# Kernel optimization log

Measured on AMD Instinct MI355X. Metric: run time of the kernel, lower is better.

## Reference

```python
import math
import jax, jax.numpy as jnp
import numpy as np

D_MODEL = 256
NUM_HEAD = 8
NUM_LEVEL = 1
KERNEL = 5
NUM_POINT = KERNEL * KERNEL
NUM_VAR = 5  # with_rotation=True
HEAD_DIM = D_MODEL // NUM_HEAD


def _kernel_indices(k=KERNEL):
    # odd kernel: linspace(-(k-1)/2, (k-1)/2, k); torch.meshgrid default 'ij'; stack([j,i])/k
    idx = jnp.linspace(-(k - 1) / 2.0, (k - 1) / 2.0, k)
    ii, jj = jnp.meshgrid(idx, idx, indexing='ij')
    return jnp.stack([jj, ii], axis=-1).reshape(-1, 2) / k  # (P, 2)


def setup_inputs() -> dict:
    key = jax.random.key(0)
    ks = jax.random.split(key, 8)
    B, LQ = 2, 4096
    Hf, Wf = 188, 188
    LV = Hf * Wf
    d = D_MODEL
    nb = NUM_LEVEL * NUM_HEAD * NUM_VAR
    na = NUM_HEAD * NUM_LEVEL * NUM_POINT
    return {
        'query': jax.random.normal(ks[0], (B, LQ, d), jnp.float32),
        'value': jax.random.normal(ks[1], (B, LV, d), jnp.float32),
        'ref_windows': jax.random.uniform(ks[2], (B, LQ, 7), jnp.float32),
        'W_box': jax.random.normal(ks[3], (nb, d), jnp.float32) * 0.02,
        'b_box': jax.random.uniform(ks[4], (nb,), jnp.float32),
        'W_attn': jax.random.normal(ks[5], (na, d), jnp.float32) * 0.02,
        'b_attn': jnp.zeros((na,), jnp.float32),
        'W_value': jax.random.normal(ks[6], (d, d), jnp.float32) * 0.02,
        'b_value': jnp.zeros((d,), jnp.float32),
        'W_out': jax.random.normal(ks[7], (d, d), jnp.float32) * 0.02,
        'b_out': jnp.zeros((d,), jnp.float32),
        'H_feat': Hf,
        'W_feat': Wf,
    }


def reference(query, value, ref_windows, W_box, b_box, W_attn, b_attn,
              W_value, b_value, W_out, b_out, H_feat, W_feat):
    B, LQ, d = query.shape
    LV = value.shape[1]
    Hh, Lv, P, Dh = NUM_HEAD, NUM_LEVEL, NUM_POINT, HEAD_DIM

    # value projection -> (B, LV, Hh, Dh)
    v = (value @ W_value.T + b_value).reshape(B, LV, Hh, Dh)

    # attention weights: softmax over (level*point) per head
    attn = jax.nn.softmax((query @ W_attn.T + b_attn).reshape(B, LQ, Hh, Lv * P), axis=-1)
    attn = attn.reshape(B, LQ, Hh, Lv, P)

    # --- _where_to_attend ---
    ob = (query @ W_box.T + b_box).reshape(B, LQ, Hh, Lv, NUM_VAR)
    rw = ref_windows[:, :, None, None, :]                    # (B,LQ,1,1,7)
    ref_boxes = rw[..., jnp.array([0, 1, 3, 4])]             # cx, cy, w, h
    ref_angles = rw[..., 6:7]
    off_boxes, off_angles = ob[..., :4], ob[..., 4:5]
    angles = (ref_angles + off_angles / 16.0) * (2.0 * math.pi)
    boxes = ref_boxes + off_boxes / 8.0 * ref_boxes[..., jnp.array([2, 3, 2, 3])]
    center = boxes[..., None, :2]                            # (B,LQ,Hh,Lv,1,2)
    size = boxes[..., None, 2:4]
    cos_a, sin_a = jnp.cos(angles), jnp.sin(angles)
    rot = jnp.stack([cos_a, -sin_a, sin_a, cos_a], axis=-1).reshape(B, LQ, Hh, Lv, 1, 2, 2)
    g = _kernel_indices() * jax.nn.relu(size)                # (B,LQ,Hh,Lv,P,2)
    grid = center + (g[..., None, :] * rot).sum(-1)          # (B,LQ,Hh,Lv,P,2), normalized [0,1]

    # --- single-level bilinear sampling (align_corners=False, zero padding) ---
    gl = grid[:, :, :, 0]                                    # (B,LQ,Hh,P,2)
    gx = gl[..., 0] * W_feat - 0.5
    gy = gl[..., 1] * H_feat - 0.5
    x0 = jnp.floor(gx)
    y0 = jnp.floor(gy)
    x0i = x0.astype(jnp.int32)
    y0i = y0.astype(jnp.int32)
    wx1 = gx - x0
    wy1 = gy - y0
    wx0 = 1.0 - wx1
    wy0 = 1.0 - wy1

    b_idx = jnp.arange(B)[:, None, None, None]
    h_idx = jnp.arange(Hh)[None, None, :, None]

    def gather(yi, xi):
        valid = (xi >= 0) & (xi < W_feat) & (yi >= 0) & (yi < H_feat)
        lin = jnp.clip(yi, 0, H_feat - 1) * W_feat + jnp.clip(xi, 0, W_feat - 1)
        return v[b_idx, lin, h_idx] * valid[..., None]       # (B,LQ,Hh,P,Dh)

    s = (gather(y0i, x0i) * (wy0 * wx0)[..., None]
         + gather(y0i, x0i + 1) * (wy0 * wx1)[..., None]
         + gather(y0i + 1, x0i) * (wy1 * wx0)[..., None]
         + gather(y0i + 1, x0i + 1) * (wy1 * wx1)[..., None])

    out_heads = (s * attn[:, :, :, 0, :, None]).sum(axis=3)  # (B,LQ,Hh,Dh)
    out = out_heads.reshape(B, LQ, Hh * Dh) @ W_out.T + b_out
    attn_w = attn.reshape(B, LQ, Hh, Lv, KERNEL, KERNEL)
    return out, attn_w
```

## Files before the change

kernel.cpp:

```cpp
#include <hip/hip_runtime.h>


typedef float floatx4 __attribute__((ext_vector_type(4)));
typedef short shortx8 __attribute__((ext_vector_type(8)));

static __device__ __forceinline__ unsigned short f2bf(float x) {
    unsigned int u = __float_as_uint(x);
    return (unsigned short)((u + 0x7fffu + ((u >> 16) & 1u)) >> 16);
}
static __device__ __forceinline__ unsigned int pack2(float a, float b) {
    return (unsigned int)f2bf(a) | ((unsigned int)f2bf(b) << 16);
}
static __device__ __forceinline__ void async16(const void* g, void* lds) {
    __builtin_amdgcn_global_load_lds(
        (const __attribute__((address_space(1))) unsigned int*)g,
        (__attribute__((address_space(3))) unsigned int*)lds, 16, 0, 0);
}

__global__ __launch_bounds__(256) void convert_kernel(
    const float* __restrict__ W_value, unsigned short* __restrict__ wvbf,
    const float* __restrict__ W_attn, const float* __restrict__ W_box,
    float* __restrict__ Wab,
    const float* __restrict__ W_out, unsigned short* __restrict__ wobf,
    const float* __restrict__ b_attn, const float* __restrict__ b_box,
    float* __restrict__ bab)
{
    const int blk = blockIdx.x, tid = threadIdx.x;
    if (blk < 16) {
        int base = blk * 1024 + tid;
#pragma unroll
        for (int k = 0; k < 4; ++k) {
            int j = base + k * 256;
            float4 f = ((const float4*)W_value)[j];
            ((uint2*)wvbf)[j] = make_uint2(pack2(f.x, f.y), pack2(f.z, f.w));
        }
    } else if (blk < 32) {
        int base = (blk - 16) * 1024 + tid;
#pragma unroll
        for (int k = 0; k < 4; ++k) {
            int j = base + k * 256;
            int row = j >> 6, col = (j & 63) * 4;
            float4 f;
            if (row < 200)      f = *(const float4*)(W_attn + (size_t)row * 256 + col);
            else if (row < 240) f = *(const float4*)(W_box + (size_t)(row - 200) * 256 + col);
            else                f = make_float4(0.f, 0.f, 0.f, 0.f);
            ((float4*)Wab)[j] = f;
        }
    } else if (blk < 48) {
        int base = (blk - 32) * 1024 + tid;
#pragma unroll
        for (int k = 0; k < 4; ++k) {
            int j = base + k * 256;
            float4 f = ((const float4*)W_out)[j];
            ((uint2*)wobf)[j] = make_uint2(pack2(f.x, f.y), pack2(f.z, f.w));
        }
    } else {
        bab[tid] = tid < 200 ? b_attn[tid] : (tid < 240 ? b_box[tid - 200] : 0.f);
    }
}

__global__ __launch_bounds__(512) void gemm_vproj(
    const float* __restrict__ A,
    const unsigned short* __restrict__ Bw,
    const float* __restrict__ bias,
    unsigned short* __restrict__ Vout, int M, int LV)
{
    __shared__ unsigned short Bres[256 * 256];
    __shared__ unsigned short As[2][64 * 64];
    const int tid = threadIdx.x;
    const int wv = tid >> 6, lane = tid & 63;
    const int lr = lane & 15, lq = lane >> 4;
    const int wm = wv & 1, wn = wv >> 1;
    const int rowA = tid >> 3;
    const int gA = tid & 7;
    const int gAsw = gA ^ (rowA & 7);

#pragma unroll
    for (int j = 0; j < 16; ++j) {
        int G = j * 512 + tid;
        int row = G >> 5, g = G & 31;
        async16(Bw + (size_t)row * 256 + (g ^ (row & 7)) * 8,
                (char*)Bres + j * 8192 + wv * 1024);
    }

    const int niter = (M + 63) / 64;
    const int stride = gridDim.x;

    int it0 = blockIdx.x;
    float4 pf0, pf1;
    {
        int ra = it0 * 64 + rowA; ra = ra < M ? ra : M - 1;
        const float* ap = A + (size_t)ra * 256 + gA * 8;
        pf0 = *(const float4*)ap; pf1 = *(const float4*)(ap + 4);
        uint4 pv = make_uint4(pack2(pf0.x, pf0.y), pack2(pf0.z, pf0.w),
                              pack2(pf1.x, pf1.y), pack2(pf1.z, pf1.w));
        *(uint4*)((char*)As[0] + rowA * 128 + gAsw * 16) = pv;
    }
    __syncthreads();

    int buf = 0;
    for (int it = it0; it < niter; it += stride) {
        const int m0 = it * 64;
        floatx4 acc[2][4];
#pragma unroll
        for (int i = 0; i < 2; ++i)
#pragma unroll
            for (int j = 0; j < 4; ++j) acc[i][j] = (floatx4){0.f, 0.f, 0.f, 0.f};

#pragma unroll
        for (int kc = 0; kc < 4; ++kc) {
            int nit = it, nkc = kc + 1;
            if (nkc == 4) { nkc = 0; nit = it + stride; if (nit >= niter) nit = it; }
            {
                int ra = nit * 64 + rowA; ra = ra < M ? ra : M - 1;
                const float* ap = A + (size_t)ra * 256 + nkc * 64 + gA * 8;
                pf0 = *(const float4*)ap; pf1 = *(const float4*)(ap + 4);
            }
#pragma unroll
            for (int kb = 0; kb < 2; ++kb) {
                shortx8 af[2], bfr[4];
#pragma unroll
                for (int t = 0; t < 2; ++t) {
                    int arow = wm * 32 + t * 16 + lr;
                    af[t] = *(const shortx8*)((const char*)As[buf] + arow * 128 +
                                              (((kb * 4 + lq) ^ (arow & 7)) * 16));
                }
#pragma unroll
                for (int t = 0; t < 4; ++t) {
                    int brow = wn * 64 + t * 16 + lr;
                    int gg = kc * 8 + kb * 4 + lq;
                    bfr[t] = *(const shortx8*)((const char*)Bres + brow * 512 +
                                               ((gg ^ (brow & 7)) * 16));
                }
#pragma unroll
                for (int ti = 0; ti < 2; ++ti)
#pragma unroll
                    for (int tj = 0; tj < 4; ++tj)
                        acc[ti][tj] = __builtin_amdgcn_mfma_f32_16x16x32_bf16(bfr[tj], af[ti], acc[ti][tj], 0, 0, 0);
            }
            {
                uint4 pv = make_uint4(pack2(pf0.x, pf0.y), pack2(pf0.z, pf0.w),
                                      pack2(pf1.x, pf1.y), pack2(pf1.z, pf1.w));
                *(uint4*)((char*)As[buf ^ 1] + rowA * 128 + gAsw * 16) = pv;
            }
            __syncthreads();
            buf ^= 1;
        }
#pragma unroll
        for (int ti = 0; ti < 2; ++ti) {
            int m = m0 + wm * 32 + ti * 16 + lr;
            if (m >= M) continue;
            int b = m >= LV ? 1 : 0;
            int lv = m - (b ? LV : 0);
#pragma unroll
            for (int tj = 0; tj < 4; ++tj) {
                int nb = wn * 64 + tj * 16 + lq * 4;
                float4 bv = *(const float4*)(bias + nb);
                int h = nb >> 5, dh = nb & 31;
                unsigned short* dst = Vout + ((size_t)(b * 8 + h) * LV + lv) * 32 + dh;
                *(uint2*)dst = make_uint2(pack2(acc[ti][tj][0] + bv.x, acc[ti][tj][1] + bv.y),
                                          pack2(acc[ti][tj][2] + bv.z, acc[ti][tj][3] + bv.w));
            }
        }
    }
}

__global__ __launch_bounds__(256) void gemm_nt_bias(
    const float* __restrict__ A, const float* __restrict__ W,
    const float* __restrict__ bias, float* __restrict__ C, int M)
{
    const int K = 256, N = 256;
    __shared__ float As[16][68];
    __shared__ float Bs[16][68];
    int tid = threadIdx.x;
    int tcol = tid & 15, trow = tid >> 4;
    int m0 = blockIdx.x * 64, n0 = blockIdx.y * 64;
    int lr = tid >> 2, lc = (tid & 3) << 2;
    float acc[4][4] = {};
    for (int k0 = 0; k0 < K; k0 += 16) {
        int arow = m0 + lr; if (arow > M - 1) arow = M - 1;
        float4 av = *(const float4*)(A + (size_t)arow * K + k0 + lc);
        float4 wv = *(const float4*)(W + (size_t)(n0 + lr) * K + k0 + lc);
        __syncthreads();
        As[lc + 0][lr] = av.x; As[lc + 1][lr] = av.y; As[lc + 2][lr] = av.z; As[lc + 3][lr] = av.w;
        Bs[lc + 0][lr] = wv.x; Bs[lc + 1][lr] = wv.y; Bs[lc + 2][lr] = wv.z; Bs[lc + 3][lr] = wv.w;
        __syncthreads();
#pragma unroll
        for (int k = 0; k < 16; ++k) {
            float4 a4 = *(const float4*)&As[k][trow << 2];
            float4 b4 = *(const float4*)&Bs[k][tcol << 2];
            float a[4] = {a4.x, a4.y, a4.z, a4.w};
            float bb[4] = {b4.x, b4.y, b4.z, b4.w};
#pragma unroll
            for (int i = 0; i < 4; i++)
#pragma unroll
                for (int j = 0; j < 4; j++) acc[i][j] += a[i] * bb[j];
        }
    }
#pragma unroll
    for (int i = 0; i < 4; i++) {
        int m = m0 + trow * 4 + i;
        if (m >= M) continue;
#pragma unroll
        for (int j = 0; j < 4; j++) {
            int n = n0 + tcol * 4 + j;
            C[(size_t)m * N + n] = acc[i][j] + bias[n];
        }
    }
}

__global__ __launch_bounds__(256) void decode_sample_kernel(
    const unsigned short* __restrict__ v,
    const float* __restrict__ logits,
    const float* __restrict__ ref_windows,
    float* __restrict__ attn_out,
    unsigned short* __restrict__ ohbf,
    const int* __restrict__ Hf_p, const int* __restrict__ Wf_p, int LV, int LQ)
{
    __shared__ float lg[8][32];
    __shared__ float rw[8][7];
    __shared__ float prm[8][6];
    __shared__ float mxinv[8][2];
    __shared__ uint4 pk[8][25][2];

    const int lin = blockIdx.y * 16 + blockIdx.x;
    const int nc = gridDim.y;
    const int seq = lin >> 3;
    const int c = seq % nc;
    const int s = (lin & 7) + ((seq / nc) << 3);
    const int b = s >> 3, h = s & 7;
    const int tid = threadIdx.x;
    const int Hf = *Hf_p, Wf = *Wf_p;
    const size_t mbase = (size_t)b * LQ + c * 8;

    if (tid < 240) {
        int qq = tid / 30, j = tid - qq * 30;
        int col = (j < 25) ? h * 25 + j : 200 + h * 5 + (j - 25);
        lg[qq][j] = logits[(mbase + qq) * 256 + col];
    }
    if (tid < 56) {
        int qq = tid / 7, k = tid - qq * 7;
        rw[qq][k] = ref_windows[(mbase + qq) * 7 + k];
    }
    __syncthreads();

    if (tid < 8) {
        int qq = tid;
        float mx = -1e30f;
#pragma unroll
        for (int p = 0; p < 25; p++) mx = fmaxf(mx, lg[qq][p]);
        float ssum = 0.f;
#pragma unroll
        for (int p = 0; p < 25; p++) ssum += expf(lg[qq][p] - mx);
        mxinv[qq][0] = mx; mxinv[qq][1] = 1.f / ssum;
        float cx = rw[qq][0] + lg[qq][25] * 0.125f * rw[qq][3];
        float cy = rw[qq][1] + lg[qq][26] * 0.125f * rw[qq][4];
        float bw = rw[qq][3] + lg[qq][27] * 0.125f * rw[qq][3];
        float bh = rw[qq][4] + lg[qq][28] * 0.125f * rw[qq][4];
        float ang = (rw[qq][6] + lg[qq][29] * 0.0625f) * 6.283185307179586f;
        prm[qq][0] = cx; prm[qq][1] = cy;
        prm[qq][2] = fmaxf(bw, 0.f); prm[qq][3] = fmaxf(bh, 0.f);
        prm[qq][4] = cosf(ang); prm[qq][5] = sinf(ang);
    }
    __syncthreads();

    if (tid < 200) {
        int qq = tid / 25, p = tid - qq * 25;
        float a = expf(lg[qq][p] - mxinv[qq][0]) * mxinv[qq][1];
        attn_out[(mbase + qq) * 200 + h * 25 + p] = a;
        int pi = p / 5, pj = p - pi * 5;
        float g0 = (float)(pj - 2) * 0.2f * prm[qq][2];
        float g1 = (float)(pi - 2) * 0.2f * prm[qq][3];
        float ca = prm[qq][4], sa = prm[qq][5];
        float gx = (prm[qq][0] + g0 * ca - g1 * sa) * (float)Wf - 0.5f;
        float gy = (prm[qq][1] + g0 * sa + g1 * ca) * (float)Hf - 0.5f;
        float x0f = floorf(gx), y0f = floorf(gy);
        int x0 = (int)x0f, y0 = (int)y0f;
        float wx1 = gx - x0f, wy1 = gy - y0f;
        float wx0 = 1.f - wx1, wy0 = 1.f - wy1;
        int y1 = y0 + 1;
        int bx; float wl, wr;
        if (x0 >= 0 && x0 <= Wf - 2)      { bx = x0;     wl = wx0; wr = wx1; }
        else if (x0 == -1)                { bx = 0;      wl = wx1; wr = 0.f; }
        else if (x0 == Wf - 1)            { bx = Wf - 2; wl = 0.f; wr = wx0; }
        else                              { bx = 0;      wl = 0.f; wr = 0.f; }
        float wy0v = (y0 >= 0 && y0 < Hf) ? wy0 : 0.f;
        float wy1v = (y1 >= 0 && y1 < Hf) ? wy1 : 0.f;
        int cy0 = min(max(y0, 0), Hf - 1), cy1 = min(max(y1, 0), Hf - 1);
        unsigned off0 = (unsigned)(cy0 * Wf + bx) * 16u;
        unsigned off1 = (unsigned)(cy1 * Wf + bx) * 16u;
        float aw0 = a * wy0v, aw1 = a * wy1v;
        pk[qq][p][0] = make_uint4(__float_as_uint(aw0 * wl), __float_as_uint(aw1 * wl), off0, off1);
        pk[qq][p][1] = make_uint4(__float_as_uint(aw0 * wr), __float_as_uint(aw1 * wr), off0, off1);
    }
    __syncthreads();

    const int qq = tid >> 5, l = tid & 31;
    const unsigned int* vw = (const unsigned int*)(v + (size_t)s * LV * 32);
    const uint4* pkp = &pk[qq][0][l >> 4];
    float e0 = 0.f, o0 = 0.f, e1 = 0.f, o1 = 0.f;
#pragma unroll
    for (int p = 0; p < 25; ++p) {
        uint4 t = pkp[2 * p];
        float w0 = __uint_as_float(t.x), w1 = __uint_as_float(t.y);
        unsigned u0 = vw[t.z + l];
        unsigned u1 = vw[t.w + l];
        e0 += w0 * __uint_as_float(u0 << 16);
        o0 += w0 * __uint_as_float(u0 & 0xffff0000u);
        e1 += w1 * __uint_as_float(u1 << 16);
        o1 += w1 * __uint_as_float(u1 & 0xffff0000u);
    }
    float a0 = e0 + e1, a1 = o0 + o1;
    a0 += __shfl_xor(a0, 16, 32);
    a1 += __shfl_xor(a1, 16, 32);
    if (l < 16)
        ((unsigned int*)ohbf)[(mbase + qq) * 128 + h * 16 + l] = pack2(a0, a1);
}

__global__ __launch_bounds__(256) void gemm_out(
    const unsigned short* __restrict__ Ab,
    const unsigned short* __restrict__ Bw,
    const float* __restrict__ bias,
    float* __restrict__ C, int M)
{
    constexpr int BM = 64;
    constexpr int NI = BM / 32, TI = BM / 32;
    __shared__ unsigned short As[2][BM * 64];
    __shared__ unsigned short Bs[2][128 * 64];
    const int tid = threadIdx.x;
    const int wv = tid >> 6, lane = tid & 63;
    const int lr = lane & 15, lq = lane >> 4;
    const int m0 = blockIdx.x * BM, n0 = blockIdx.y * 128;
    const int wm = wv & 1, wn = wv >> 1;
    const int srow = tid >> 3;
    const int colg = tid & 7;
    const int colgSw = colg ^ (srow & 7);

    floatx4 acc[TI][4];
#pragma unroll
    for (int i = 0; i < TI; ++i)
#pragma unroll
        for (int j = 0; j < 4; ++j) acc[i][j] = (floatx4){0.f, 0.f, 0.f, 0.f};

    auto compute = [&](const unsigned short* Acur, const unsigned short* Bcur) {
#pragma unroll
        for (int kb = 0; kb < 2; ++kb) {
            shortx8 af[TI], bfr[4];
#pragma unroll
            for (int t = 0; t < TI; ++t) {
                int arow = wm * (BM / 2) + t * 16 + lr;
                af[t] = *(const shortx8*)&Acur[arow * 64 + (((kb * 4 + lq) ^ (arow & 7)) * 8)];
            }
#pragma unroll
            for (int t = 0; t < 4; ++t) {
                int brow = wn * 64 + t * 16 + lr;
                bfr[t] = *(const shortx8*)&Bcur[brow * 64 + (((kb * 4 + lq) ^ (brow & 7)) * 8)];
            }
#pragma unroll
            for (int ti = 0; ti < TI; ++ti)
#pragma unroll
                for (int tj = 0; tj < 4; ++tj)
                    acc[ti][tj] = __builtin_amdgcn_mfma_f32_16x16x32_bf16(bfr[tj], af[ti], acc[ti][tj], 0, 0, 0);
        }
    };

#pragma unroll
    for (int i = 0; i < NI; ++i) {
        int ra = m0 + i * 32 + srow; ra = ra < M ? ra : M - 1;
        async16(Ab + (size_t)ra * 256 + colgSw * 8, (char*)As[0] + i * 4096 + wv * 1024);
    }
#pragma unroll
    for (int i = 0; i < 4; ++i) {
        int rb = n0 + i * 32 + srow;
        async16(Bw + (size_t)rb * 256 + colgSw * 8, (char*)Bs[0] + i * 4096 + wv * 1024);
    }
    __syncthreads();
    int cur = 0;
    for (int kc = 0; kc < 4; ++kc) {
        const int nk = (kc + 1) * 64;
        if (kc < 3) {
#pragma unroll
            for (int i = 0; i < NI; ++i) {
                int ra = m0 + i * 32 + srow; ra = ra < M ? ra : M - 1;
                async16(Ab + (size_t)ra * 256 + nk + colgSw * 8,
                        (char*)As[cur ^ 1] + i * 4096 + wv * 1024);
            }
#pragma unroll
            for (int i = 0; i < 4; ++i) {
                int rb = n0 + i * 32 + srow;
                async16(Bw + (size_t)rb * 256 + nk + colgSw * 8,
                        (char*)Bs[cur ^ 1] + i * 4096 + wv * 1024);
            }
        }
        compute(As[cur], Bs[cur]);
        __syncthreads();
        cur ^= 1;
    }
#pragma unroll
    for (int ti = 0; ti < TI; ++ti) {
        int m = m0 + wm * (BM / 2) + ti * 16 + lr;
        if (m >= M) continue;
        float* Crow = C + (size_t)m * 256;
#pragma unroll
        for (int tj = 0; tj < 4; ++tj) {
            int nb = n0 + wn * 64 + tj * 16 + lq * 4;
            float4 bv = *(const float4*)(bias + nb);
            float4 o = make_float4(acc[ti][tj][0] + bv.x, acc[ti][tj][1] + bv.y,
                                   acc[ti][tj][2] + bv.z, acc[ti][tj][3] + bv.w);
            *(float4*)(Crow + nb) = o;
        }
    }
}

extern "C" void kernel_launch(void* const* d_in, const int* in_sizes, int n_in,
                              void* d_out, int out_size, void* d_ws, size_t ws_size,
                              hipStream_t stream) {
    const float* query       = (const float*)d_in[0];
    const float* value       = (const float*)d_in[1];
    const float* ref_windows = (const float*)d_in[2];
    const float* W_box       = (const float*)d_in[3];
    const float* b_box       = (const float*)d_in[4];
    const float* W_attn      = (const float*)d_in[5];
    const float* b_attn      = (const float*)d_in[6];
    const float* W_value     = (const float*)d_in[7];
    const float* b_value     = (const float*)d_in[8];
    const float* W_out       = (const float*)d_in[9];
    const float* b_out       = (const float*)d_in[10];
    const int*   Hf          = (const int*)d_in[11];
    const int*   Wf          = (const int*)d_in[12];

    const int M1 = in_sizes[1] / 256;
    const int MQ = in_sizes[0] / 256;
    const int LQ = MQ / 2;
    const int LV = M1 / 2;

    unsigned short* Vout = (unsigned short*)d_ws;
    unsigned short* ohbf = Vout + (size_t)M1 * 256;
    unsigned short* wvbf = ohbf + (size_t)MQ * 256;
    unsigned short* wobf = wvbf + 65536;
    float* Wab       = (float*)(wobf + 65536);
    float* bab       = Wab + 65536;
    float* logits    = bab + 256;

    float* out0     = (float*)d_out;
    float* attn_out = out0 + (size_t)MQ * 256;

    convert_kernel<<<49, 256, 0, stream>>>(W_value, wvbf, W_attn, W_box, Wab,
                                           W_out, wobf, b_attn, b_box, bab);
    gemm_vproj<<<256, 512, 0, stream>>>(value, wvbf, b_value, Vout, M1, LV);
    dim3 g2(MQ / 64, 4);
    gemm_nt_bias<<<g2, 256, 0, stream>>>(query, Wab, bab, logits, MQ);
    decode_sample_kernel<<<dim3(16, LQ / 8), 256, 0, stream>>>(
        Vout, logits, ref_windows, attn_out, ohbf, Hf, Wf, LV, LQ);
    dim3 g4(MQ / 64, 2);
    gemm_out<<<g4, 256, 0, stream>>>(ohbf, wobf, b_out, out0, MQ);
}
```

Before: 216.4 us.

## Fuse logits GEMM into weight-prep kernel and widen value projection blocks to 1024 threads

The query logits GEMM now runs inside the weight-conversion kernel, reading W_attn/W_box directly with inline bias selection. This removes one launch and the intermediate Wab/bab buffers. The value-projection GEMM moves from 512 to 1024 threads per block, with each wave owning a 16-row slice and loading half as much A per thread. That raises the number of waves per block but lowers per-wave MFMA work and A-fragment reuse. Prep blocks are heterogeneous, and MQ is assumed to be 128 tiles of 64 rows.

New measurement: 220.2 us. No clear change (+1.8%).

```diff
diff --git a/kernel.cpp b/kernel.cpp
--- a/kernel.cpp
+++ b/kernel.cpp
@@ -17,49 +17,78 @@
         (__attribute__((address_space(3))) unsigned int*)lds, 16, 0, 0);
 }
 
-__global__ __launch_bounds__(256) void convert_kernel(
+__global__ __launch_bounds__(256) void prep_kernel(
+    const float* __restrict__ query,
+    const float* __restrict__ W_attn, const float* __restrict__ W_box,
+    const float* __restrict__ b_attn, const float* __restrict__ b_box,
+    float* __restrict__ logits, int MQ,
     const float* __restrict__ W_value, unsigned short* __restrict__ wvbf,
-    const float* __restrict__ W_attn, const float* __restrict__ W_box,
-    float* __restrict__ Wab,
-    const float* __restrict__ W_out, unsigned short* __restrict__ wobf,
-    const float* __restrict__ b_attn, const float* __restrict__ b_box,
-    float* __restrict__ bab)
+    const float* __restrict__ W_out, unsigned short* __restrict__ wobf)
 {
     const int blk = blockIdx.x, tid = threadIdx.x;
-    if (blk < 16) {
-        int base = blk * 1024 + tid;
+    if (blk < 512) {
+        const int K = 256, N = 256, M = MQ;
+        __shared__ float As[16][68];
+        __shared__ float Bs[16][68];
+        int tcol = tid & 15, trow = tid >> 4;
+        int m0 = (blk & 127) * 64, n0 = (blk >> 7) * 64;
+        int lr = tid >> 2, lc = (tid & 3) << 2;
+        float acc[4][4] = {};
+        for (int k0 = 0; k0 < K; k0 += 16) {
+            int arow = m0 + lr; if (arow > M - 1) arow = M - 1;
+            float4 av = *(const float4*)(query + (size_t)arow * K + k0 + lc);
+            int r = n0 + lr;
+            float4 wv;
+            if (r < 200)      wv = *(const float4*)(W_attn + (size_t)r * 256 + k0 + lc);
+            else if (r < 240) wv = *(const float4*)(W_box + (size_t)(r - 200) * 256 + k0 + lc);
+            else              wv = make_float4(0.f, 0.f, 0.f, 0.f);
+            __syncthreads();
+            As[lc + 0][lr] = av.x; As[lc + 1][lr] = av.y; As[lc + 2][lr] = av.z; As[lc + 3][lr] = av.w;
+            Bs[lc + 0][lr] = wv.x; Bs[lc + 1][lr] = wv.y; Bs[lc + 2][lr] = wv.z; Bs[lc + 3][lr] = wv.w;
+            __syncthreads();
+#pragma unroll
+            for (int k = 0; k < 16; ++k) {
+                float4 a4 = *(const float4*)&As[k][trow << 2];
+                float4 b4 = *(const float4*)&Bs[k][tcol << 2];
+                float a[4] = {a4.x, a4.y, a4.z, a4.w};
+                float bb[4] = {b4.x, b4.y, b4.z, b4.w};
+#pragma unroll
+                for (int i = 0; i < 4; i++)
+#pragma unroll
+                    for (int j = 0; j < 4; j++) acc[i][j] += a[i] * bb[j];
+            }
+        }
+#pragma unroll
+        for (int i = 0; i < 4; i++) {
+            int m = m0 + trow * 4 + i;
+            if (m >= M) continue;
+#pragma unroll
+            for (int j = 0; j < 4; j++) {
+                int n = n0 + tcol * 4 + j;
+                float bb = n < 200 ? b_attn[n] : (n < 240 ? b_box[n - 200] : 0.f);
+                logits[(size_t)m * N + n] = acc[i][j] + bb;
+            }
+        }
+    } else if (blk < 528) {
+        int base = (blk - 512) * 1024 + tid;
 #pragma unroll
         for (int k = 0; k < 4; ++k) {
             int j = base + k * 256;
             float4 f = ((const float4*)W_value)[j];
             ((uint2*)wvbf)[j] = make_uint2(pack2(f.x, f.y), pack2(f.z, f.w));
         }
-    } else if (blk < 32) {
-        int base = (blk - 16) * 1024 + tid;
-#pragma unroll
-        for (int k = 0; k < 4; ++k) {
-            int j = base + k * 256;
-            int row = j >> 6, col = (j & 63) * 4;
-            float4 f;
-            if (row < 200)      f = *(const float4*)(W_attn + (size_t)row * 256 + col);
-            else if (row < 240) f = *(const float4*)(W_box + (size_t)(row - 200) * 256 + col);
-            else                f = make_float4(0.f, 0.f, 0.f, 0.f);
-            ((float4*)Wab)[j] = f;
-        }
-    } else if (blk < 48) {
-        int base = (blk - 32) * 1024 + tid;
+    } else {
+        int base = (blk - 528) * 1024 + tid;
 #pragma unroll
         for (int k = 0; k < 4; ++k) {
             int j = base + k * 256;
             float4 f = ((const float4*)W_out)[j];
             ((uint2*)wobf)[j] = make_uint2(pack2(f.x, f.y), pack2(f.z, f.w));
         }
-    } else {
-        bab[tid] = tid < 200 ? b_attn[tid] : (tid < 240 ? b_box[tid - 200] : 0.f);
-    }
-}
-
-__global__ __launch_bounds__(512) void gemm_vproj(
+    }
+}
+
+__global__ __launch_bounds__(1024) void gemm_vproj(
     const float* __restrict__ A,
     const unsigned short* __restrict__ Bw,
     const float* __restrict__ bias,
@@ -70,42 +99,37 @@
     const int tid = threadIdx.x;
     const int wv = tid >> 6, lane = tid & 63;
     const int lr = lane & 15, lq = lane >> 4;
-    const int wm = wv & 1, wn = wv >> 1;
-    const int rowA = tid >> 3;
-    const int gA = tid & 7;
-    const int gAsw = gA ^ (rowA & 7);
-
-#pragma unroll
-    for (int j = 0; j < 16; ++j) {
-        int G = j * 512 + tid;
+    const int wm = wv & 3, wn = wv >> 2;
+    const int rowA = tid >> 4;
+    const int gA4 = tid & 15;
+    const int dstA = rowA * 128 + (((gA4 >> 1) ^ (rowA & 7)) * 16) + (gA4 & 1) * 8;
+
+#pragma unroll
+    for (int j = 0; j < 8; ++j) {
+        int G = j * 1024 + tid;
         int row = G >> 5, g = G & 31;
         async16(Bw + (size_t)row * 256 + (g ^ (row & 7)) * 8,
-                (char*)Bres + j * 8192 + wv * 1024);
+                (char*)Bres + j * 16384 + wv * 1024);
     }
 
     const int niter = (M + 63) / 64;
     const int stride = gridDim.x;
 
     int it0 = blockIdx.x;
-    float4 pf0, pf1;
+    float4 pf;
     {
         int ra = it0 * 64 + rowA; ra = ra < M ? ra : M - 1;
-        const float* ap = A + (size_t)ra * 256 + gA * 8;
-        pf0 = *(const float4*)ap; pf1 = *(const float4*)(ap + 4);
-        uint4 pv = make_uint4(pack2(pf0.x, pf0.y), pack2(pf0.z, pf0.w),
-                              pack2(pf1.x, pf1.y), pack2(pf1.z, pf1.w));
-        *(uint4*)((char*)As[0] + rowA * 128 + gAsw * 16) = pv;
+        pf = *(const float4*)(A + (size_t)ra * 256 + gA4 * 4);
+        *(uint2*)((char*)As[0] + dstA) = make_uint2(pack2(pf.x, pf.y), pack2(pf.z, pf.w));
     }
     __syncthreads();
 
     int buf = 0;
     for (int it = it0; it < niter; it += stride) {
         const int m0 = it * 64;
-        floatx4 acc[2][4];
-#pragma unroll
-        for (int i = 0; i < 2; ++i)
-#pragma unroll
-            for (int j = 0; j < 4; ++j) acc[i][j] = (floatx4){0.f, 0.f, 0.f, 0.f};
+        floatx4 acc[4];
+#pragma unroll
+        for (int j = 0; j < 4; ++j) acc[j] = (floatx4){0.f, 0.f, 0.f, 0.f};
 
 #pragma unroll
         for (int kc = 0; kc < 4; ++kc) {
@@ -113,17 +137,15 @@
             if (nkc == 4) { nkc = 0; nit = it + stride; if (nit >= niter) nit = it; }
             {
                 int ra = nit * 64 + rowA; ra = ra < M ? ra : M - 1;
-                const float* ap = A + (size_t)ra * 256 + nkc * 64 + gA * 8;
-                pf0 = *(const float4*)ap; pf1 = *(const float4*)(ap + 4);
+                pf = *(const float4*)(A + (size_t)ra * 256 + nkc * 64 + gA4 * 4);
             }
 #pragma unroll
             for (int kb = 0; kb < 2; ++kb) {
-                shortx8 af[2], bfr[4];
-#pragma unroll
-                for (int t = 0; t < 2; ++t) {
-                    int arow = wm * 32 + t * 16 + lr;
-                    af[t] = *(const shortx8*)((const char*)As[buf] + arow * 128 +
-                                              (((kb * 4 + lq) ^ (arow & 7)) * 16));
+                shortx8 af, bfr[4];
+                {
+                    int arow = wm * 16 + lr;
+                    af = *(const shortx8*)((const char*)As[buf] + arow * 128 +
+                                           (((kb * 4 + lq) ^ (arow & 7)) * 16));
                 }
 #pragma unroll
                 for (int t = 0; t < 4; ++t) {
@@ -133,78 +155,28 @@
                                                ((gg ^ (brow & 7)) * 16));
                 }
 #pragma unroll
-                for (int ti = 0; ti < 2; ++ti)
-#pragma unroll
-                    for (int tj = 0; tj < 4; ++tj)
-                        acc[ti][tj] = __builtin_amdgcn_mfma_f32_16x16x32_bf16(bfr[tj], af[ti], acc[ti][tj], 0, 0, 0);
-            }
-            {
-                uint4 pv = make_uint4(pack2(pf0.x, pf0.y), pack2(pf0.z, pf0.w),
-                                      pack2(pf1.x, pf1.y), pack2(pf1.z, pf1.w));
-                *(uint4*)((char*)As[buf ^ 1] + rowA * 128 + gAsw * 16) = pv;
-            }
+                for (int tj = 0; tj < 4; ++tj)
+                    acc[tj] = __builtin_amdgcn_mfma_f32_16x16x32_bf16(bfr[tj], af, acc[tj], 0, 0, 0);
+            }
+            *(uint2*)((char*)As[buf ^ 1] + dstA) = make_uint2(pack2(pf.x, pf.y), pack2(pf.z, pf.w));
             __syncthreads();
             buf ^= 1;
         }
-#pragma unroll
-        for (int ti = 0; ti < 2; ++ti) {
-            int m = m0 + wm * 32 + ti * 16 + lr;
-            if (m >= M) continue;
-            int b = m >= LV ? 1 : 0;
-            int lv = m - (b ? LV : 0);
-#pragma unroll
-            for (int tj = 0; tj < 4; ++tj) {
-                int nb = wn * 64 + tj * 16 + lq * 4;
-                float4 bv = *(const float4*)(bias + nb);
-                int h = nb >> 5, dh = nb & 31;
-                unsigned short* dst = Vout + ((size_t)(b * 8 + h) * LV + lv) * 32 + dh;
-                *(uint2*)dst = make_uint2(pack2(acc[ti][tj][0] + bv.x, acc[ti][tj][1] + bv.y),
-                                          pack2(acc[ti][tj][2] + bv.z, acc[ti][tj][3] + bv.w));
-            }
-        }
-    }
-}
-
-__global__ __launch_bounds__(256) void gemm_nt_bias(
-    const float* __restrict__ A, const float* __restrict__ W,
-    const float* __restrict__ bias, float* __restrict__ C, int M)
-{
-    const int K = 256, N = 256;
-    __shared__ float As[16][68];
-    __shared__ float Bs[16][68];
-    int tid = threadIdx.x;
-    int tcol = tid & 15, trow = tid >> 4;
-    int m0 = blockIdx.x * 64, n0 = blockIdx.y * 64;
-    int lr = tid >> 2, lc = (tid & 3) << 2;
-    float acc[4][4] = {};
-    for (int k0 = 0; k0 < K; k0 += 16) {
-        int arow = m0 + lr; if (arow > M - 1) arow = M - 1;
-        float4 av = *(const float4*)(A + (size_t)arow * K + k0 + lc);
-        float4 wv = *(const float4*)(W + (size_t)(n0 + lr) * K + k0 + lc);
-        __syncthreads();
-        As[lc + 0][lr] = av.x; As[lc + 1][lr] = av.y; As[lc + 2][lr] = av.z; As[lc + 3][lr] = av.w;
-        Bs[lc + 0][lr] = wv.x; Bs[lc + 1][lr] = wv.y; Bs[lc + 2][lr] = wv.z; Bs[lc + 3][lr] = wv.w;
-        __syncthreads();
-#pragma unroll
-        for (int k = 0; k < 16; ++k) {
-            float4 a4 = *(const float4*)&As[k][trow << 2];
-            float4 b4 = *(const float4*)&Bs[k][tcol << 2];
-            float a[4] = {a4.x, a4.y, a4.z, a4.w};
-            float bb[4] = {b4.x, b4.y, b4.z, b4.w};
-#pragma unroll
-            for (int i = 0; i < 4; i++)
-#pragma unroll
-                for (int j = 0; j < 4; j++) acc[i][j] += a[i] * bb[j];
-        }
-    }
-#pragma unroll
-    for (int i = 0; i < 4; i++) {
-        int m = m0 + trow * 4 + i;
-        if (m >= M) continue;
-#pragma unroll
-        for (int j = 0; j < 4; j++) {
-            int n = n0 + tcol * 4 + j;
-            C[(size_t)m * N + n] = acc[i][j] + bias[n];
+        {
+            int m = m0 + wm * 16 + lr;
+            if (m < M) {
+                int b = m >= LV ? 1 : 0;
+                int lv = m - (b ? LV : 0);
+#pragma unroll
+                for (int tj = 0; tj < 4; ++tj) {
+                    int nb = wn * 64 + tj * 16 + lq * 4;
+                    float4 bv = *(const float4*)(bias + nb);
+                    int h = nb >> 5, dh = nb & 31;
+                    unsigned short* dst = Vout + ((size_t)(b * 8 + h) * LV + lv) * 32 + dh;
+                    *(uint2*)dst = make_uint2(pack2(acc[tj][0] + bv.x, acc[tj][1] + bv.y),
+                                              pack2(acc[tj][2] + bv.z, acc[tj][3] + bv.w));
+                }
+            }
         }
     }
 }
@@ -438,18 +410,14 @@
     unsigned short* ohbf = Vout + (size_t)M1 * 256;
     unsigned short* wvbf = ohbf + (size_t)MQ * 256;
     unsigned short* wobf = wvbf + 65536;
-    float* Wab       = (float*)(wobf + 65536);
-    float* bab       = Wab + 65536;
-    float* logits    = bab + 256;
+    float* logits    = (float*)(wobf + 65536);
 
     float* out0     = (float*)d_out;
     float* attn_out = out0 + (size_t)MQ * 256;
 
-    convert_kernel<<<49, 256, 0, stream>>>(W_value, wvbf, W_attn, W_box, Wab,
-                                           W_out, wobf, b_attn, b_box, bab);
-    gemm_vproj<<<256, 512, 0, stream>>>(value, wvbf, b_value, Vout, M1, LV);
-    dim3 g2(MQ / 64, 4);
-    gemm_nt_bias<<<g2, 256, 0, stream>>>(query, Wab, bab, logits, MQ);
+    prep_kernel<<<544, 256, 0, stream>>>(query, W_attn, W_box, b_attn, b_box,
+                                         logits, MQ, W_value, wvbf, W_out, wobf);
+    gemm_vproj<<<256, 1024, 0, stream>>>(value, wvbf, b_value, Vout, M1, LV);
     decode_sample_kernel<<<dim3(16, LQ / 8), 256, 0, stream>>>(
         Vout, logits, ref_windows, attn_out, ohbf, Hf, Wf, LV, LQ);
     dim3 g4(MQ / 64, 2);
```

## Fuse query logits GEMM into prep kernel and widen decode blocks to 16 queries

Applied to the files above, without the earlier changes.

The query-side logits GEMM now runs inside the weight-conversion prep kernel. It reads W_attn, W_box and the biases directly, so the separate Wab/bab staging buffers and one kernel launch are gone. The decode/sample kernel now handles 16 queries per block with 512 threads instead of 8 with 256, which halves the grid and amortises per-block setup. The value projection now has to wait for the larger prep kernel, since the logits GEMM blocks share it with the W_value conversion. The decode kernel also uses more shared memory per block.

Result: no change. 218.7 us (+1.1%).

```diff
diff --git a/kernel.cpp b/kernel.cpp
--- a/kernel.cpp
+++ b/kernel.cpp
@@ -17,45 +17,74 @@
         (__attribute__((address_space(3))) unsigned int*)lds, 16, 0, 0);
 }
 
-__global__ __launch_bounds__(256) void convert_kernel(
+__global__ __launch_bounds__(256) void prep_kernel(
+    const float* __restrict__ query,
+    const float* __restrict__ W_attn, const float* __restrict__ W_box,
+    const float* __restrict__ b_attn, const float* __restrict__ b_box,
+    float* __restrict__ logits, int MQ,
     const float* __restrict__ W_value, unsigned short* __restrict__ wvbf,
-    const float* __restrict__ W_attn, const float* __restrict__ W_box,
-    float* __restrict__ Wab,
-    const float* __restrict__ W_out, unsigned short* __restrict__ wobf,
-    const float* __restrict__ b_attn, const float* __restrict__ b_box,
-    float* __restrict__ bab)
+    const float* __restrict__ W_out, unsigned short* __restrict__ wobf)
 {
     const int blk = blockIdx.x, tid = threadIdx.x;
-    if (blk < 16) {
-        int base = blk * 1024 + tid;
+    if (blk < 512) {
+        const int K = 256, N = 256, M = MQ;
+        __shared__ float As[16][68];
+        __shared__ float Bs[16][68];
+        int tcol = tid & 15, trow = tid >> 4;
+        int m0 = (blk & 127) * 64, n0 = (blk >> 7) * 64;
+        int lr = tid >> 2, lc = (tid & 3) << 2;
+        float acc[4][4] = {};
+        for (int k0 = 0; k0 < K; k0 += 16) {
+            int arow = m0 + lr; if (arow > M - 1) arow = M - 1;
+            float4 av = *(const float4*)(query + (size_t)arow * K + k0 + lc);
+            int r = n0 + lr;
+            float4 wv;
+            if (r < 200)      wv = *(const float4*)(W_attn + (size_t)r * 256 + k0 + lc);
+            else if (r < 240) wv = *(const float4*)(W_box + (size_t)(r - 200) * 256 + k0 + lc);
+            else              wv = make_float4(0.f, 0.f, 0.f, 0.f);
+            __syncthreads();
+            As[lc + 0][lr] = av.x; As[lc + 1][lr] = av.y; As[lc + 2][lr] = av.z; As[lc + 3][lr] = av.w;
+            Bs[lc + 0][lr] = wv.x; Bs[lc + 1][lr] = wv.y; Bs[lc + 2][lr] = wv.z; Bs[lc + 3][lr] = wv.w;
+            __syncthreads();
+#pragma unroll
+            for (int k = 0; k < 16; ++k) {
+                float4 a4 = *(const float4*)&As[k][trow << 2];
+                float4 b4 = *(const float4*)&Bs[k][tcol << 2];
+                float a[4] = {a4.x, a4.y, a4.z, a4.w};
+                float bb[4] = {b4.x, b4.y, b4.z, b4.w};
+#pragma unroll
+                for (int i = 0; i < 4; i++)
+#pragma unroll
+                    for (int j = 0; j < 4; j++) acc[i][j] += a[i] * bb[j];
+            }
+        }
+#pragma unroll
+        for (int i = 0; i < 4; i++) {
+            int m = m0 + trow * 4 + i;
+            if (m >= M) continue;
+#pragma unroll
+            for (int j = 0; j < 4; j++) {
+                int n = n0 + tcol * 4 + j;
+                float bb = n < 200 ? b_attn[n] : (n < 240 ? b_box[n - 200] : 0.f);
+                logits[(size_t)m * N + n] = acc[i][j] + bb;
+            }
+        }
+    } else if (blk < 528) {
+        int base = (blk - 512) * 1024 + tid;
 #pragma unroll
         for (int k = 0; k < 4; ++k) {
             int j = base + k * 256;
             float4 f = ((const float4*)W_value)[j];
             ((uint2*)wvbf)[j] = make_uint2(pack2(f.x, f.y), pack2(f.z, f.w));
         }
-    } else if (blk < 32) {
-        int base = (blk - 16) * 1024 + tid;
-#pragma unroll
-        for (int k = 0; k < 4; ++k) {
-            int j = base + k * 256;
-            int row = j >> 6, col = (j & 63) * 4;
-            float4 f;
-            if (row < 200)      f = *(const float4*)(W_attn + (size_t)row * 256 + col);
-            else if (row < 240) f = *(const float4*)(W_box + (size_t)(row - 200) * 256 + col);
-            else                f = make_float4(0.f, 0.f, 0.f, 0.f);
-            ((float4*)Wab)[j] = f;
-        }
-    } else if (blk < 48) {
-        int base = (blk - 32) * 1024 + tid;
+    } else {
+        int base = (blk - 528) * 1024 + tid;
 #pragma unroll
         for (int k = 0; k < 4; ++k) {
             int j = base + k * 256;
             float4 f = ((const float4*)W_out)[j];
             ((uint2*)wobf)[j] = make_uint2(pack2(f.x, f.y), pack2(f.z, f.w));
         }
-    } else {
-        bab[tid] = tid < 200 ? b_attn[tid] : (tid < 240 ? b_box[tid - 200] : 0.f);
     }
 }
 
@@ -165,51 +194,7 @@
     }
 }
 
-__global__ __launch_bounds__(256) void gemm_nt_bias(
-    const float* __restrict__ A, const float* __restrict__ W,
-    const float* __restrict__ bias, float* __restrict__ C, int M)
-{
-    const int K = 256, N = 256;
-    __shared__ float As[16][68];
-    __shared__ float Bs[16][68];
-    int tid = threadIdx.x;
-    int tcol = tid & 15, trow = tid >> 4;
-    int m0 = blockIdx.x * 64, n0 = blockIdx.y * 64;
-    int lr = tid >> 2, lc = (tid & 3) << 2;
-    float acc[4][4] = {};
-    for (int k0 = 0; k0 < K; k0 += 16) {
-        int arow = m0 + lr; if (arow > M - 1) arow = M - 1;
-        float4 av = *(const float4*)(A + (size_t)arow * K + k0 + lc);
-        float4 wv = *(const float4*)(W + (size_t)(n0 + lr) * K + k0 + lc);
-        __syncthreads();
-        As[lc + 0][lr] = av.x; As[lc + 1][lr] = av.y; As[lc + 2][lr] = av.z; As[lc + 3][lr] = av.w;
-        Bs[lc + 0][lr] = wv.x; Bs[lc + 1][lr] = wv.y; Bs[lc + 2][lr] = wv.z; Bs[lc + 3][lr] = wv.w;
-        __syncthreads();
-#pragma unroll
-        for (int k = 0; k < 16; ++k) {
-            float4 a4 = *(const float4*)&As[k][trow << 2];
-            float4 b4 = *(const float4*)&Bs[k][tcol << 2];
-            float a[4] = {a4.x, a4.y, a4.z, a4.w};
-            float bb[4] = {b4.x, b4.y, b4.z, b4.w};
-#pragma unroll
-            for (int i = 0; i < 4; i++)
-#pragma unroll
-                for (int j = 0; j < 4; j++) acc[i][j] += a[i] * bb[j];
-        }
-    }
-#pragma unroll
-    for (int i = 0; i < 4; i++) {
-        int m = m0 + trow * 4 + i;
-        if (m >= M) continue;
-#pragma unroll
-        for (int j = 0; j < 4; j++) {
-            int n = n0 + tcol * 4 + j;
-            C[(size_t)m * N + n] = acc[i][j] + bias[n];
-        }
-    }
-}
-
-__global__ __launch_bounds__(256) void decode_sample_kernel(
+__global__ __launch_bounds__(512) void decode_sample_kernel(
     const unsigned short* __restrict__ v,
     const float* __restrict__ logits,
     const float* __restrict__ ref_windows,
@@ -217,11 +202,11 @@
     unsigned short* __restrict__ ohbf,
     const int* __restrict__ Hf_p, const int* __restrict__ Wf_p, int LV, int LQ)
 {
-    __shared__ float lg[8][32];
-    __shared__ float rw[8][7];
-    __shared__ float prm[8][6];
-    __shared__ float mxinv[8][2];
-    __shared__ uint4 pk[8][25][2];
+    __shared__ float lg[16][32];
+    __shared__ float rw[16][7];
+    __shared__ float prm[16][6];
+    __shared__ float mxinv[16][2];
+    __shared__ uint4 pk[16][25][2];
 
     const int lin = blockIdx.y * 16 + blockIdx.x;
     const int nc = gridDim.y;
@@ -231,20 +216,20 @@
     const int b = s >> 3, h = s & 7;
     const int tid = threadIdx.x;
     const int Hf = *Hf_p, Wf = *Wf_p;
-    const size_t mbase = (size_t)b * LQ + c * 8;
-
-    if (tid < 240) {
+    const size_t mbase = (size_t)b * LQ + c * 16;
+
+    if (tid < 480) {
         int qq = tid / 30, j = tid - qq * 30;
         int col = (j < 25) ? h * 25 + j : 200 + h * 5 + (j - 25);
         lg[qq][j] = logits[(mbase + qq) * 256 + col];
     }
-    if (tid < 56) {
+    if (tid < 112) {
         int qq = tid / 7, k = tid - qq * 7;
         rw[qq][k] = ref_windows[(mbase + qq) * 7 + k];
     }
     __syncthreads();
 
-    if (tid < 8) {
+    if (tid < 16) {
         int qq = tid;
         float mx = -1e30f;
 #pragma unroll
@@ -264,7 +249,7 @@
     }
     __syncthreads();
 
-    if (tid < 200) {
+    if (tid < 400) {
         int qq = tid / 25, p = tid - qq * 25;
         float a = expf(lg[qq][p] - mxinv[qq][0]) * mxinv[qq][1];
         attn_out[(mbase + qq) * 200 + h * 25 + p] = a;
@@ -438,19 +423,15 @@
     unsigned short* ohbf = Vout + (size_t)M1 * 256;
     unsigned short* wvbf = ohbf + (size_t)MQ * 256;
     unsigned short* wobf = wvbf + 65536;
-    float* Wab       = (float*)(wobf + 65536);
-    float* bab       = Wab + 65536;
-    float* logits    = bab + 256;
+    float* logits    = (float*)(wobf + 65536);
 
     float* out0     = (float*)d_out;
     float* attn_out = out0 + (size_t)MQ * 256;
 
-    convert_kernel<<<49, 256, 0, stream>>>(W_value, wvbf, W_attn, W_box, Wab,
-                                           W_out, wobf, b_attn, b_box, bab);
+    prep_kernel<<<544, 256, 0, stream>>>(query, W_attn, W_box, b_attn, b_box,
+                                         logits, MQ, W_value, wvbf, W_out, wobf);
     gemm_vproj<<<256, 512, 0, stream>>>(value, wvbf, b_value, Vout, M1, LV);
-    dim3 g2(MQ / 64, 4);
-    gemm_nt_bias<<<g2, 256, 0, stream>>>(query, Wab, bab, logits, MQ);
-    decode_sample_kernel<<<dim3(16, LQ / 8), 256, 0, stream>>>(
+    decode_sample_kernel<<<dim3(16, LQ / 16), 512, 0, stream>>>(
         Vout, logits, ref_windows, attn_out, ohbf, Hf, Wf, LV, LQ);
     dim3 g4(MQ / 64, 2);
     gemm_out<<<g4, 256, 0, stream>>>(ohbf, wobf, b_out, out0, MQ);
```
